# Kernel optimization log

Hardware: AMD Instinct MI355X
Metric: run time of the kernel (lower is better)

The kernel has to match this reference:

```python
import jax, jax.numpy as jnp
import numpy as np

N = 100000   # relation nodes (== source nodes per scale)
D = 128      # per-scale feature size
EPS = 1e-6   # LayerNorm eps from the torch module


def setup_inputs() -> dict:
    key = jax.random.key(0)
    ks = jax.random.split(key, 10)
    inp = {}
    for i, s in enumerate(['s1', 's2', 's3', 's4']):
        inp[f'feat_{s}'] = jax.random.normal(ks[i], (N, D), dtype=jnp.float32)
        inp[f'idx_{s}'] = jax.random.randint(ks[4 + i], (N,), 0, N, dtype=jnp.int32)
    inp['W'] = jax.random.normal(ks[8], (4 * D, 4 * D), dtype=jnp.float32) * 0.04
    inp['b'] = jnp.zeros((4 * D,), dtype=jnp.float32)
    inp['gamma'] = jnp.ones((4 * D,), dtype=jnp.float32)
    inp['beta'] = jnp.zeros((4 * D,), dtype=jnp.float32)
    return inp


def reference(feat_s1, feat_s2, feat_s3, feat_s4,
              idx_s1, idx_s2, idx_s3, idx_s4,
              W, b, gamma, beta):
    # copy_src message passing per scale == gather src features to each
    # relation node (uniform in-degree 1), mailbox flatten -> [N, D] per scale.
    gathered = jnp.concatenate([
        jnp.take(feat_s1, idx_s1, axis=0),
        jnp.take(feat_s2, idx_s2, axis=0),
        jnp.take(feat_s3, idx_s3, axis=0),
        jnp.take(feat_s4, idx_s4, axis=0),
    ], axis=1)                                  # [N, 4D]
    h = gathered @ W.T + b                      # nn.Linear(4D, 4D)
    h = jax.nn.relu(h)
    # LayerNorm(4D, eps=1e-6, elementwise_affine=True)
    mu = jnp.mean(h, axis=-1, keepdims=True)
    var = jnp.mean(jnp.square(h - mu), axis=-1, keepdims=True)
    return (h - mu) * jax.lax.rsqrt(var + EPS) * gamma + beta
```

## Files before the change

kernel.cpp:

```cpp
#include <hip/hip_runtime.h>
#include <stdint.h>

#define N_ROWS 100000
#define EPS 1e-6f

typedef float f32x4 __attribute__((ext_vector_type(4)));
typedef __bf16 bf16x8 __attribute__((ext_vector_type(8)));

__device__ __forceinline__ ushort f2bf(float f) {
  union { float f; uint32_t u; } v; v.f = f;
  uint32_t u = v.u;
  return (ushort)((u + 0x7FFFu + ((u >> 16) & 1u)) >> 16);
}

__global__ __launch_bounds__(256) void wconv2_kernel(const float* __restrict__ W,
                                                     ushort* __restrict__ Wf) {
  int t = blockIdx.x * 256 + threadIdx.x;
  int frag = t >> 6;
  int lane = t & 63;
  int j = (frag >> 4) * 16 + (lane & 15);
  int kb = (frag & 15) * 32 + (lane >> 4) * 8;
  const float* src = W + j * 512 + kb;
  float4 a = *(const float4*)src;
  float4 b = *(const float4*)(src + 4);
  ushort4 lo, hi;
  lo.x = f2bf(a.x); lo.y = f2bf(a.y); lo.z = f2bf(a.z); lo.w = f2bf(a.w);
  hi.x = f2bf(b.x); hi.y = f2bf(b.y); hi.z = f2bf(b.z); hi.w = f2bf(b.w);
  ushort* dst = Wf + (size_t)t * 8;
  *(ushort4*)dst = lo;
  *(ushort4*)(dst + 4) = hi;
}

__global__ __launch_bounds__(512, 4) void fused2_kernel(
    const float* __restrict__ f1, const float* __restrict__ f2,
    const float* __restrict__ f3, const float* __restrict__ f4,
    const int* __restrict__ i1, const int* __restrict__ i2,
    const int* __restrict__ i3, const int* __restrict__ i4,
    const ushort* __restrict__ Wf, const float* __restrict__ bias,
    const float* __restrict__ gamma, const float* __restrict__ beta,
    float* __restrict__ out) {
  __shared__ ushort Al[2][64 * 32];
  __shared__ float2 red[64 * 8];

  const int t = threadIdx.x;
  const int w = t >> 6;
  const int l = t & 63;
  const int cl = l & 15;
  const int gq = l >> 4;
  const int blk = blockIdx.x;

  const int arow = t >> 3;
  const int e8 = t & 7;
  int gi = blk * 64 + arow;
  int gic = gi < N_ROWS ? gi : (N_ROWS - 1);
  const float* ap0 = f1 + (size_t)i1[gic] * 128 + e8 * 4;
  const float* ap1 = f2 + (size_t)i2[gic] * 128 + e8 * 4;
  const float* ap2 = f3 + (size_t)i3[gic] * 128 + e8 * 4;
  const float* ap3 = f4 + (size_t)i4[gic] * 128 + e8 * 4;
  const int achunk = (e8 >> 1) ^ ((arow >> 1) & 3);
  const int awoff = arow * 32 + achunk * 8 + (e8 & 1) * 4;
  const int roff = cl * 32 + ((gq ^ ((cl >> 1) & 3)) * 8);

  const ushort* Bbase = Wf + (size_t)w * 4 * 8192 + (size_t)l * 8;

  f32x4 acc[4][4];
#pragma unroll
  for (int rb = 0; rb < 4; ++rb)
#pragma unroll
    for (int cb = 0; cb < 4; ++cb)
      acc[rb][cb] = (f32x4){0.f, 0.f, 0.f, 0.f};

  {
    float4 av = *(const float4*)ap0;
    ushort4 ab;
    ab.x = f2bf(av.x); ab.y = f2bf(av.y); ab.z = f2bf(av.z); ab.w = f2bf(av.w);
    *(ushort4*)(Al[0] + awoff) = ab;
  }
  __syncthreads();

#pragma unroll
  for (int kt = 0; kt < 16; ++kt) {
    const int cur = kt & 1;
    float4 av;
    if (kt < 15) {
      const int t2 = (kt + 1) >> 2;
      const int k2 = (kt + 1) & 3;
      const float* ap = (t2 == 0) ? ap0 : (t2 == 1) ? ap1 : (t2 == 2) ? ap2 : ap3;
      av = *(const float4*)(ap + k2 * 32);
    }
    bf16x8 bfr[4];
#pragma unroll
    for (int cb = 0; cb < 4; ++cb)
      bfr[cb] = *(const bf16x8*)(Bbase + cb * 8192 + kt * 512);
    bf16x8 af[4];
#pragma unroll
    for (int rb = 0; rb < 4; ++rb)
      af[rb] = *(const bf16x8*)(Al[cur] + rb * 512 + roff);
#pragma unroll
    for (int cb = 0; cb < 4; ++cb)
#pragma unroll
      for (int rb = 0; rb < 4; ++rb)
        acc[rb][cb] = __builtin_amdgcn_mfma_f32_16x16x32_bf16(
            af[rb], bfr[cb], acc[rb][cb], 0, 0, 0);
    if (kt < 15) {
      ushort4 ab;
      ab.x = f2bf(av.x); ab.y = f2bf(av.y); ab.z = f2bf(av.z); ab.w = f2bf(av.w);
      *(ushort4*)(Al[cur ^ 1] + awoff) = ab;
    }
    __syncthreads();
  }

  const int wcol = w * 64;
  float bia[4], gam[4], bet[4];
#pragma unroll
  for (int cb = 0; cb < 4; ++cb) {
    int col = wcol + cb * 16 + cl;
    bia[cb] = bias[col];
    gam[cb] = gamma[col];
    bet[cb] = beta[col];
  }

#pragma unroll
  for (int rb = 0; rb < 4; ++rb) {
#pragma unroll
    for (int r = 0; r < 4; ++r) {
      float s = 0.f, ss = 0.f;
#pragma unroll
      for (int cb = 0; cb < 4; ++cb) {
        float v = acc[rb][cb][r] + bia[cb];
        v = fmaxf(v, 0.f);
        acc[rb][cb][r] = v;
        s += v;
        ss += v * v;
      }
#pragma unroll
      for (int m = 1; m < 16; m <<= 1) {
        s += __shfl_xor(s, m);
        ss += __shfl_xor(ss, m);
      }
      if (cl == 0) {
        int row = rb * 16 + gq * 4 + r;
        red[row * 8 + w] = make_float2(s, ss);
      }
    }
  }
  __syncthreads();

#pragma unroll
  for (int rb = 0; rb < 4; ++rb) {
#pragma unroll
    for (int r = 0; r < 4; ++r) {
      int row = rb * 16 + gq * 4 + r;
      float S = 0.f, SS = 0.f;
#pragma unroll
      for (int wv = 0; wv < 8; ++wv) {
        float2 p = red[row * 8 + wv];
        S += p.x;
        SS += p.y;
      }
      float mu = S * (1.f / 512.f);
      float var = SS * (1.f / 512.f) - mu * mu;
      float rstd = rsqrtf(var + EPS);
      int g = blk * 64 + row;
      if (g < N_ROWS) {
        float* orow = out + (size_t)g * 512 + wcol;
#pragma unroll
        for (int cb = 0; cb < 4; ++cb)
          orow[cb * 16 + cl] = (acc[rb][cb][r] - mu) * rstd * gam[cb] + bet[cb];
      }
    }
  }
}

extern "C" void kernel_launch(void* const* d_in, const int* in_sizes, int n_in,
                              void* d_out, int out_size, void* d_ws, size_t ws_size,
                              hipStream_t stream) {
  const float* f1 = (const float*)d_in[0];
  const int* i1 = (const int*)d_in[1];
  const float* f2 = (const float*)d_in[2];
  const int* i2 = (const int*)d_in[3];
  const float* f3 = (const float*)d_in[4];
  const int* i3 = (const int*)d_in[5];
  const float* f4 = (const float*)d_in[6];
  const int* i4 = (const int*)d_in[7];
  const float* W = (const float*)d_in[8];
  const float* b = (const float*)d_in[9];
  const float* gm = (const float*)d_in[10];
  const float* bt = (const float*)d_in[11];
  float* out = (float*)d_out;
  ushort* Wf = (ushort*)d_ws;

  wconv2_kernel<<<128, 256, 0, stream>>>(W, Wf);
  fused2_kernel<<<(N_ROWS + 63) / 64, 512, 0, stream>>>(
      f1, f2, f3, f4, i1, i2, i3, i4, Wf, b, gm, bt, out);
}
```

Before: 159.7 us.

## Stage full 128-wide scale slices in LDS per sync and use nontemporal output stores

The A-tile pipeline now loads an entire 128-column scale slice (four float4 per thread) per stage instead of one 32-column slice. This cuts the number of __syncthreads barriers from 16 to 4 and puts more gather loads in flight at once. The LDS buffer grows fourfold and uses a new XOR swizzle, which adds LDS pressure and registers. Output stores become nontemporal to avoid polluting cache with the large write stream.

Result: faster. 153.4 us (-3.9%).

```diff
diff --git a/kernel.cpp b/kernel.cpp
--- a/kernel.cpp
+++ b/kernel.cpp
@@ -31,7 +31,7 @@
   *(ushort4*)(dst + 4) = hi;
 }
 
-__global__ __launch_bounds__(512, 4) void fused2_kernel(
+__global__ __launch_bounds__(512, 4) void fused3_kernel(
     const float* __restrict__ f1, const float* __restrict__ f2,
     const float* __restrict__ f3, const float* __restrict__ f4,
     const int* __restrict__ i1, const int* __restrict__ i2,
@@ -39,7 +39,7 @@
     const ushort* __restrict__ Wf, const float* __restrict__ bias,
     const float* __restrict__ gamma, const float* __restrict__ beta,
     float* __restrict__ out) {
-  __shared__ ushort Al[2][64 * 32];
+  __shared__ ushort Al[2][64 * 128];
   __shared__ float2 red[64 * 8];
 
   const int t = threadIdx.x;
@@ -57,11 +57,13 @@
   const float* ap1 = f2 + (size_t)i2[gic] * 128 + e8 * 4;
   const float* ap2 = f3 + (size_t)i3[gic] * 128 + e8 * 4;
   const float* ap3 = f4 + (size_t)i4[gic] * 128 + e8 * 4;
-  const int achunk = (e8 >> 1) ^ ((arow >> 1) & 3);
-  const int awoff = arow * 32 + achunk * 8 + (e8 & 1) * 4;
-  const int roff = cl * 32 + ((gq ^ ((cl >> 1) & 3)) * 8);
-
-  const ushort* Bbase = Wf + (size_t)w * 4 * 8192 + (size_t)l * 8;
+
+  int wboff[4];
+#pragma unroll
+  for (int q = 0; q < 4; ++q)
+    wboff[q] = arow * 128 + (((q * 4) | (e8 >> 1)) ^ (arow & 15)) * 8 + (e8 & 1) * 4;
+
+  const ushort* Bbase = Wf + ((size_t)w * 4 * 16 * 64 + l) * 8;
 
   f32x4 acc[4][4];
 #pragma unroll
@@ -71,41 +73,56 @@
       acc[rb][cb] = (f32x4){0.f, 0.f, 0.f, 0.f};
 
   {
-    float4 av = *(const float4*)ap0;
-    ushort4 ab;
-    ab.x = f2bf(av.x); ab.y = f2bf(av.y); ab.z = f2bf(av.z); ab.w = f2bf(av.w);
-    *(ushort4*)(Al[0] + awoff) = ab;
+    float4 pv[4];
+#pragma unroll
+    for (int q = 0; q < 4; ++q) pv[q] = *(const float4*)(ap0 + q * 32);
+#pragma unroll
+    for (int q = 0; q < 4; ++q) {
+      ushort4 ab;
+      ab.x = f2bf(pv[q].x); ab.y = f2bf(pv[q].y);
+      ab.z = f2bf(pv[q].z); ab.w = f2bf(pv[q].w);
+      *(ushort4*)(Al[0] + wboff[q]) = ab;
+    }
   }
   __syncthreads();
 
 #pragma unroll
-  for (int kt = 0; kt < 16; ++kt) {
-    const int cur = kt & 1;
-    float4 av;
-    if (kt < 15) {
-      const int t2 = (kt + 1) >> 2;
-      const int k2 = (kt + 1) & 3;
-      const float* ap = (t2 == 0) ? ap0 : (t2 == 1) ? ap1 : (t2 == 2) ? ap2 : ap3;
-      av = *(const float4*)(ap + k2 * 32);
-    }
-    bf16x8 bfr[4];
-#pragma unroll
-    for (int cb = 0; cb < 4; ++cb)
-      bfr[cb] = *(const bf16x8*)(Bbase + cb * 8192 + kt * 512);
-    bf16x8 af[4];
-#pragma unroll
-    for (int rb = 0; rb < 4; ++rb)
-      af[rb] = *(const bf16x8*)(Al[cur] + rb * 512 + roff);
-#pragma unroll
-    for (int cb = 0; cb < 4; ++cb)
-#pragma unroll
-      for (int rb = 0; rb < 4; ++rb)
-        acc[rb][cb] = __builtin_amdgcn_mfma_f32_16x16x32_bf16(
-            af[rb], bfr[cb], acc[rb][cb], 0, 0, 0);
-    if (kt < 15) {
-      ushort4 ab;
-      ab.x = f2bf(av.x); ab.y = f2bf(av.y); ab.z = f2bf(av.z); ab.w = f2bf(av.w);
-      *(ushort4*)(Al[cur ^ 1] + awoff) = ab;
+  for (int T = 0; T < 4; ++T) {
+    const ushort* Acur = Al[T & 1];
+    float4 nv[4];
+    if (T < 3) {
+      const float* ap = (T == 0) ? ap1 : (T == 1) ? ap2 : ap3;
+#pragma unroll
+      for (int q = 0; q < 4; ++q) nv[q] = *(const float4*)(ap + q * 32);
+    }
+#pragma unroll
+    for (int kt = 0; kt < 4; ++kt) {
+      bf16x8 bfr[4];
+#pragma unroll
+      for (int cb = 0; cb < 4; ++cb)
+        bfr[cb] = *(const bf16x8*)(Bbase + ((size_t)cb * 16 + T * 4 + kt) * 512);
+      bf16x8 af[4];
+#pragma unroll
+      for (int rb = 0; rb < 4; ++rb) {
+        const int chunk = ((kt * 4) | gq) ^ cl;
+        af[rb] = *(const bf16x8*)(Acur + (rb * 16 + cl) * 128 + chunk * 8);
+      }
+#pragma unroll
+      for (int cb = 0; cb < 4; ++cb)
+#pragma unroll
+        for (int rb = 0; rb < 4; ++rb)
+          acc[rb][cb] = __builtin_amdgcn_mfma_f32_16x16x32_bf16(
+              af[rb], bfr[cb], acc[rb][cb], 0, 0, 0);
+    }
+    if (T < 3) {
+      ushort* Anx = Al[(T & 1) ^ 1];
+#pragma unroll
+      for (int q = 0; q < 4; ++q) {
+        ushort4 ab;
+        ab.x = f2bf(nv[q].x); ab.y = f2bf(nv[q].y);
+        ab.z = f2bf(nv[q].z); ab.w = f2bf(nv[q].w);
+        *(ushort4*)(Anx + wboff[q]) = ab;
+      }
     }
     __syncthreads();
   }
@@ -165,8 +182,10 @@
       if (g < N_ROWS) {
         float* orow = out + (size_t)g * 512 + wcol;
 #pragma unroll
-        for (int cb = 0; cb < 4; ++cb)
-          orow[cb * 16 + cl] = (acc[rb][cb][r] - mu) * rstd * gam[cb] + bet[cb];
+        for (int cb = 0; cb < 4; ++cb) {
+          float v = (acc[rb][cb][r] - mu) * rstd * gam[cb] + bet[cb];
+          __builtin_nontemporal_store(v, &orow[cb * 16 + cl]);
+        }
       }
     }
   }
@@ -191,6 +210,6 @@
   ushort* Wf = (ushort*)d_ws;
 
   wconv2_kernel<<<128, 256, 0, stream>>>(W, Wf);
-  fused2_kernel<<<(N_ROWS + 63) / 64, 512, 0, stream>>>(
+  fused3_kernel<<<(N_ROWS + 63) / 64, 512, 0, stream>>>(
       f1, f2, f3, f4, i1, i2, i3, i4, Wf, b, gm, bt, out);
 }
```

## Stage full gathered A tile in LDS upfront and drop per-k-step barriers

Applied to the files above, without the earlier changes.

Instead of double-buffering 32-wide K slices of the gathered activations with a barrier every step, each thread issues all its gather loads at once (16 float4 per thread), converts them to bf16 and writes the whole 64x512 A tile into LDS with an XOR swizzle. A single barrier then precedes a barrier-free MFMA loop over all 16 k-steps. This exposes more memory-level parallelism for the random gathers and removes 16 synchronisations. In exchange LDS use grows to about 64 KB per block, which may cut the number of resident blocks per CU, and raises register pressure.

Result: slower. 174.2 us (+9.1%).

```diff
diff --git a/kernel.cpp b/kernel.cpp
--- a/kernel.cpp
+++ b/kernel.cpp
@@ -6,6 +6,7 @@
 
 typedef float f32x4 __attribute__((ext_vector_type(4)));
 typedef __bf16 bf16x8 __attribute__((ext_vector_type(8)));
+typedef ushort u16x8 __attribute__((ext_vector_type(8)));
 
 __device__ __forceinline__ ushort f2bf(float f) {
   union { float f; uint32_t u; } v; v.f = f;
@@ -31,7 +32,7 @@
   *(ushort4*)(dst + 4) = hi;
 }
 
-__global__ __launch_bounds__(512, 4) void fused2_kernel(
+__global__ __launch_bounds__(512, 4) void fused4_kernel(
     const float* __restrict__ f1, const float* __restrict__ f2,
     const float* __restrict__ f3, const float* __restrict__ f4,
     const int* __restrict__ i1, const int* __restrict__ i2,
@@ -39,7 +40,7 @@
     const ushort* __restrict__ Wf, const float* __restrict__ bias,
     const float* __restrict__ gamma, const float* __restrict__ beta,
     float* __restrict__ out) {
-  __shared__ ushort Al[2][64 * 32];
+  __shared__ ushort Al[64 * 512];
   __shared__ float2 red[64 * 8];
 
   const int t = threadIdx.x;
@@ -53,15 +54,38 @@
   const int e8 = t & 7;
   int gi = blk * 64 + arow;
   int gic = gi < N_ROWS ? gi : (N_ROWS - 1);
-  const float* ap0 = f1 + (size_t)i1[gic] * 128 + e8 * 4;
-  const float* ap1 = f2 + (size_t)i2[gic] * 128 + e8 * 4;
-  const float* ap2 = f3 + (size_t)i3[gic] * 128 + e8 * 4;
-  const float* ap3 = f4 + (size_t)i4[gic] * 128 + e8 * 4;
-  const int achunk = (e8 >> 1) ^ ((arow >> 1) & 3);
-  const int awoff = arow * 32 + achunk * 8 + (e8 & 1) * 4;
-  const int roff = cl * 32 + ((gq ^ ((cl >> 1) & 3)) * 8);
-
-  const ushort* Bbase = Wf + (size_t)w * 4 * 8192 + (size_t)l * 8;
+  const float* tb0 = f1 + (size_t)i1[gic] * 128 + e8 * 8;
+  const float* tb1 = f2 + (size_t)i2[gic] * 128 + e8 * 8;
+  const float* tb2 = f3 + (size_t)i3[gic] * 128 + e8 * 8;
+  const float* tb3 = f4 + (size_t)i4[gic] * 128 + e8 * 8;
+
+  float4 pa[4][2], pb[4][2];
+#pragma unroll
+  for (int h = 0; h < 2; ++h) {
+    pa[0][h] = *(const float4*)(tb0 + h * 64);
+    pb[0][h] = *(const float4*)(tb0 + h * 64 + 4);
+    pa[1][h] = *(const float4*)(tb1 + h * 64);
+    pb[1][h] = *(const float4*)(tb1 + h * 64 + 4);
+    pa[2][h] = *(const float4*)(tb2 + h * 64);
+    pb[2][h] = *(const float4*)(tb2 + h * 64 + 4);
+    pa[3][h] = *(const float4*)(tb3 + h * 64);
+    pb[3][h] = *(const float4*)(tb3 + h * 64 + 4);
+  }
+
+#pragma unroll
+  for (int T = 0; T < 4; ++T)
+#pragma unroll
+    for (int h = 0; h < 2; ++h) {
+      u16x8 o;
+      o[0] = f2bf(pa[T][h].x); o[1] = f2bf(pa[T][h].y);
+      o[2] = f2bf(pa[T][h].z); o[3] = f2bf(pa[T][h].w);
+      o[4] = f2bf(pb[T][h].x); o[5] = f2bf(pb[T][h].y);
+      o[6] = f2bf(pb[T][h].z); o[7] = f2bf(pb[T][h].w);
+      const int c = (T * 16 + h * 8 + e8) ^ (arow & 15);
+      *(u16x8*)(Al + arow * 512 + c * 8) = o;
+    }
+
+  const ushort* Bbase = Wf + ((size_t)w * 4 * 16 * 64 + l) * 8;
 
   f32x4 acc[4][4];
 #pragma unroll
@@ -70,44 +94,26 @@
     for (int cb = 0; cb < 4; ++cb)
       acc[rb][cb] = (f32x4){0.f, 0.f, 0.f, 0.f};
 
-  {
-    float4 av = *(const float4*)ap0;
-    ushort4 ab;
-    ab.x = f2bf(av.x); ab.y = f2bf(av.y); ab.z = f2bf(av.z); ab.w = f2bf(av.w);
-    *(ushort4*)(Al[0] + awoff) = ab;
-  }
   __syncthreads();
 
 #pragma unroll
   for (int kt = 0; kt < 16; ++kt) {
-    const int cur = kt & 1;
-    float4 av;
-    if (kt < 15) {
-      const int t2 = (kt + 1) >> 2;
-      const int k2 = (kt + 1) & 3;
-      const float* ap = (t2 == 0) ? ap0 : (t2 == 1) ? ap1 : (t2 == 2) ? ap2 : ap3;
-      av = *(const float4*)(ap + k2 * 32);
-    }
     bf16x8 bfr[4];
 #pragma unroll
     for (int cb = 0; cb < 4; ++cb)
-      bfr[cb] = *(const bf16x8*)(Bbase + cb * 8192 + kt * 512);
+      bfr[cb] = *(const bf16x8*)(Bbase + ((size_t)cb * 16 + kt) * 512);
     bf16x8 af[4];
 #pragma unroll
-    for (int rb = 0; rb < 4; ++rb)
-      af[rb] = *(const bf16x8*)(Al[cur] + rb * 512 + roff);
+    for (int rb = 0; rb < 4; ++rb) {
+      const int c = (kt * 4 + gq) ^ cl;
+      af[rb] = *(const bf16x8*)(Al + (rb * 16 + cl) * 512 + c * 8);
+    }
 #pragma unroll
     for (int cb = 0; cb < 4; ++cb)
 #pragma unroll
       for (int rb = 0; rb < 4; ++rb)
         acc[rb][cb] = __builtin_amdgcn_mfma_f32_16x16x32_bf16(
             af[rb], bfr[cb], acc[rb][cb], 0, 0, 0);
-    if (kt < 15) {
-      ushort4 ab;
-      ab.x = f2bf(av.x); ab.y = f2bf(av.y); ab.z = f2bf(av.z); ab.w = f2bf(av.w);
-      *(ushort4*)(Al[cur ^ 1] + awoff) = ab;
-    }
-    __syncthreads();
   }
 
   const int wcol = w * 64;
@@ -191,6 +197,6 @@
   ushort* Wf = (ushort*)d_ws;
 
   wconv2_kernel<<<128, 256, 0, stream>>>(W, Wf);
-  fused2_kernel<<<(N_ROWS + 63) / 64, 512, 0, stream>>>(
+  fused4_kernel<<<(N_ROWS + 63) / 64, 512, 0, stream>>>(
       f1, f2, f3, f4, i1, i2, i3, i4, Wf, b, gm, bt, out);
 }
```

## Split gather into separate bf16 fragment-packing kernel before GEMM+LayerNorm

Applied to the files above, without the earlier changes.

Adds a pack kernel that gathers the four scales' rows, converts them to bf16 and writes them into a workspace laid out exactly as MFMA A-fragments. A separate GEMM+LayerNorm kernel then reads A fragments straight from global memory, dropping the LDS double buffer and the per-step syncthreads. The fused kernel is kept as a fallback when the workspace is too small. The price is an extra round trip through global memory for the packed bf16 activations (about 100 MB written and read) and one more kernel launch.

New measurement: 224.6 us. 1.41x slower.

```diff
diff --git a/kernel.cpp b/kernel.cpp
--- a/kernel.cpp
+++ b/kernel.cpp
@@ -2,10 +2,12 @@
 #include <stdint.h>
 
 #define N_ROWS 100000
+#define NRB 6250
 #define EPS 1e-6f
 
 typedef float f32x4 __attribute__((ext_vector_type(4)));
 typedef __bf16 bf16x8 __attribute__((ext_vector_type(8)));
+typedef ushort u16x8 __attribute__((ext_vector_type(8)));
 
 __device__ __forceinline__ ushort f2bf(float f) {
   union { float f; uint32_t u; } v; v.f = f;
@@ -31,6 +33,142 @@
   *(ushort4*)(dst + 4) = hi;
 }
 
+__global__ __launch_bounds__(256) void pack_kernel(
+    const float* __restrict__ f1, const float* __restrict__ f2,
+    const float* __restrict__ f3, const float* __restrict__ f4,
+    const int* __restrict__ i1, const int* __restrict__ i2,
+    const int* __restrict__ i3, const int* __restrict__ i4,
+    ushort* __restrict__ Af) {
+  const int rb = blockIdx.x;
+  const int t = threadIdx.x;
+  const int w = t >> 6;
+  const int l = t & 63;
+  const int cl = l & 15;
+  const int gq = l >> 4;
+  const int row = rb * 16 + cl;
+  const float* ft = (w == 0) ? f1 : (w == 1) ? f2 : (w == 2) ? f3 : f4;
+  const int* it = (w == 0) ? i1 : (w == 1) ? i2 : (w == 2) ? i3 : i4;
+  const float* src = ft + (size_t)it[row] * 128 + gq * 8;
+  ushort* dst = Af + ((size_t)(rb * 16 + w * 4) * 64 + l) * 8;
+#pragma unroll
+  for (int i = 0; i < 4; ++i) {
+    float4 a = *(const float4*)(src + i * 32);
+    float4 b = *(const float4*)(src + i * 32 + 4);
+    u16x8 o;
+    o[0] = f2bf(a.x); o[1] = f2bf(a.y); o[2] = f2bf(a.z); o[3] = f2bf(a.w);
+    o[4] = f2bf(b.x); o[5] = f2bf(b.y); o[6] = f2bf(b.z); o[7] = f2bf(b.w);
+    *(u16x8*)(dst + i * 512) = o;
+  }
+}
+
+__global__ __launch_bounds__(512, 3) void gemmln_kernel(
+    const ushort* __restrict__ Af, const ushort* __restrict__ Wf,
+    const float* __restrict__ bias, const float* __restrict__ gamma,
+    const float* __restrict__ beta, float* __restrict__ out) {
+  __shared__ float2 red[64 * 8];
+
+  const int t = threadIdx.x;
+  const int w = t >> 6;
+  const int l = t & 63;
+  const int cl = l & 15;
+  const int gq = l >> 4;
+  const int blk = blockIdx.x;
+
+  const ushort* Ab[4];
+#pragma unroll
+  for (int rb = 0; rb < 4; ++rb) {
+    int r4 = blk * 4 + rb;
+    if (r4 > NRB - 1) r4 = NRB - 1;
+    Ab[rb] = Af + ((size_t)r4 * 8192 + (size_t)l * 8);
+  }
+  const ushort* Bb = Wf + ((size_t)(w * 4) * 8192 + (size_t)l * 8);
+
+  f32x4 acc[4][4];
+#pragma unroll
+  for (int rb = 0; rb < 4; ++rb)
+#pragma unroll
+    for (int cb = 0; cb < 4; ++cb)
+      acc[rb][cb] = (f32x4){0.f, 0.f, 0.f, 0.f};
+
+#pragma unroll
+  for (int kt = 0; kt < 16; ++kt) {
+    bf16x8 bfr[4], af[4];
+#pragma unroll
+    for (int cb = 0; cb < 4; ++cb)
+      bfr[cb] = *(const bf16x8*)(Bb + ((size_t)(cb * 16 + kt)) * 512);
+#pragma unroll
+    for (int rb = 0; rb < 4; ++rb)
+      af[rb] = *(const bf16x8*)(Ab[rb] + (size_t)kt * 512);
+#pragma unroll
+    for (int cb = 0; cb < 4; ++cb)
+#pragma unroll
+      for (int rb = 0; rb < 4; ++rb)
+        acc[rb][cb] = __builtin_amdgcn_mfma_f32_16x16x32_bf16(
+            af[rb], bfr[cb], acc[rb][cb], 0, 0, 0);
+  }
+
+  const int wcol = w * 64;
+  float bia[4], gam[4], bet[4];
+#pragma unroll
+  for (int cb = 0; cb < 4; ++cb) {
+    int col = wcol + cb * 16 + cl;
+    bia[cb] = bias[col];
+    gam[cb] = gamma[col];
+    bet[cb] = beta[col];
+  }
+
+#pragma unroll
+  for (int rb = 0; rb < 4; ++rb) {
+#pragma unroll
+    for (int r = 0; r < 4; ++r) {
+      float s = 0.f, ss = 0.f;
+#pragma unroll
+      for (int cb = 0; cb < 4; ++cb) {
+        float v = acc[rb][cb][r] + bia[cb];
+        v = fmaxf(v, 0.f);
+        acc[rb][cb][r] = v;
+        s += v;
+        ss += v * v;
+      }
+#pragma unroll
+      for (int m = 1; m < 16; m <<= 1) {
+        s += __shfl_xor(s, m);
+        ss += __shfl_xor(ss, m);
+      }
+      if (cl == 0) {
+        int row = rb * 16 + gq * 4 + r;
+        red[row * 8 + w] = make_float2(s, ss);
+      }
+    }
+  }
+  __syncthreads();
+
+#pragma unroll
+  for (int rb = 0; rb < 4; ++rb) {
+#pragma unroll
+    for (int r = 0; r < 4; ++r) {
+      int row = rb * 16 + gq * 4 + r;
+      float S = 0.f, SS = 0.f;
+#pragma unroll
+      for (int wv = 0; wv < 8; ++wv) {
+        float2 p = red[row * 8 + wv];
+        S += p.x;
+        SS += p.y;
+      }
+      float mu = S * (1.f / 512.f);
+      float var = SS * (1.f / 512.f) - mu * mu;
+      float rstd = rsqrtf(var + EPS);
+      int g = blk * 64 + row;
+      if (g < N_ROWS) {
+        float* orow = out + (size_t)g * 512 + wcol;
+#pragma unroll
+        for (int cb = 0; cb < 4; ++cb)
+          orow[cb * 16 + cl] = (acc[rb][cb][r] - mu) * rstd * gam[cb] + bet[cb];
+      }
+    }
+  }
+}
+
 __global__ __launch_bounds__(512, 4) void fused2_kernel(
     const float* __restrict__ f1, const float* __restrict__ f2,
     const float* __restrict__ f3, const float* __restrict__ f4,
@@ -60,7 +198,6 @@
   const int achunk = (e8 >> 1) ^ ((arow >> 1) & 3);
   const int awoff = arow * 32 + achunk * 8 + (e8 & 1) * 4;
   const int roff = cl * 32 + ((gq ^ ((cl >> 1) & 3)) * 8);
-
   const ushort* Bbase = Wf + (size_t)w * 4 * 8192 + (size_t)l * 8;
 
   f32x4 acc[4][4];
@@ -188,9 +325,18 @@
   const float* gm = (const float*)d_in[10];
   const float* bt = (const float*)d_in[11];
   float* out = (float*)d_out;
+
   ushort* Wf = (ushort*)d_ws;
+  const size_t WF_BYTES = 524288;
+  const size_t AF_BYTES = (size_t)NRB * 16 * 64 * 8 * 2;
+  ushort* Af = (ushort*)((char*)d_ws + WF_BYTES);
 
   wconv2_kernel<<<128, 256, 0, stream>>>(W, Wf);
-  fused2_kernel<<<(N_ROWS + 63) / 64, 512, 0, stream>>>(
-      f1, f2, f3, f4, i1, i2, i3, i4, Wf, b, gm, bt, out);
-}
+  if (ws_size >= WF_BYTES + AF_BYTES) {
+    pack_kernel<<<NRB, 256, 0, stream>>>(f1, f2, f3, f4, i1, i2, i3, i4, Af);
+    gemmln_kernel<<<(N_ROWS + 63) / 64, 512, 0, stream>>>(Af, Wf, b, gm, bt, out);
+  } else {
+    fused2_kernel<<<(N_ROWS + 63) / 64, 512, 0, stream>>>(
+        f1, f2, f3, f4, i1, i2, i3, i4, Wf, b, gm, bt, out);
+  }
+}
```
